# Kernel optimization log

Measured on AMD Instinct MI355X. Metric: run time of the kernel, lower is better.

The kernel has to match this reference:

```python
import jax, jax.numpy as jnp
import numpy as np

HEADS = 8
DIM_HEAD = 64


def setup_inputs() -> dict:
    key = jax.random.key(0)
    ks = jax.random.split(key, 5)
    B, N, C, coor = 2, 2048, 256, 3
    dim_inner = HEADS * DIM_HEAD  # 512
    # weight scale 1/16 ~ 1/sqrt(256) keeps softmax logits in a sane range
    w_scale = 1.0 / 16.0
    return {
        "x": jax.random.normal(ks[0], (B, N, C, coor), dtype=jnp.float32),
        "Wq": jax.random.normal(ks[1], (dim_inner, C), dtype=jnp.float32) * w_scale,
        "Wk": jax.random.normal(ks[2], (dim_inner, C), dtype=jnp.float32) * w_scale,
        "Wv": jax.random.normal(ks[3], (dim_inner, C), dtype=jnp.float32) * w_scale,
        "Wo": jax.random.normal(ks[4], (C, dim_inner), dtype=jnp.float32) * w_scale,
    }


def _split_heads(t, B, N, coor):
    # b n (h d) c -> b h n (d c)
    t = t.reshape(B, N, HEADS, DIM_HEAD, coor)
    t = t.transpose(0, 2, 1, 3, 4)
    return t.reshape(B, HEADS, N, DIM_HEAD * coor)


def reference(x, Wq, Wk, Wv, Wo):
    B, N, C, coor = x.shape
    # VNLinear: einsum('... i c, o i -> ... o c')
    q = jnp.einsum('bnic,oi->bnoc', x, Wq)
    k = jnp.einsum('bnic,oi->bnoc', x, Wk)
    v = jnp.einsum('bnic,oi->bnoc', x, Wv)
    q = _split_heads(q, B, N, coor)  # (B, H, N, d*c)
    k = _split_heads(k, B, N, coor)
    v = _split_heads(v, B, N, coor)
    scale = (DIM_HEAD * coor) ** -0.5
    sim = jnp.einsum('bhie,bhje->bhij', q, k) * scale  # (B, H, N, N)
    attn = jax.nn.softmax(sim, axis=-1)
    out = jnp.einsum('bhij,bhje->bhie', attn, v)  # (B, H, N, d*c)
    # b h n (d c) -> b n (h d) c
    out = out.reshape(B, HEADS, N, DIM_HEAD, coor).transpose(0, 2, 1, 3, 4)
    out = out.reshape(B, N, HEADS * DIM_HEAD, coor)
    # to_out VNLinear
    return jnp.einsum('bnic,oi->bnoc', out, Wo)  # (B, N, C, 3)
```

## Files before the change

### kernel.cpp

```cpp
#include <hip/hip_runtime.h>

#define HEADS 8
#define DH 64
#define CO 3
#define E 192
#define NSEQ 2048
#define BATCH 2
#define CIN 256
#define DINNER 512
#define NTOK 4096
#define BHTOT 16

typedef __attribute__((ext_vector_type(8))) short bf16x8;
typedef __attribute__((ext_vector_type(4))) short bf16x4;
typedef __attribute__((ext_vector_type(4))) float f32x4;
typedef __attribute__((ext_vector_type(4))) float float4v;

static __device__ inline short f2bf(float f) {
  union { float f; unsigned u; } v; v.f = f;
  unsigned r = (v.u + 0x7FFFu + ((v.u >> 16) & 1u)) >> 16;
  return (short)r;
}

static __device__ inline float bf2f(short s) {
  union { unsigned u; float f; } a;
  a.u = ((unsigned)(unsigned short)s) << 16;
  return a.f;
}

static __device__ inline void load_lds16(const short* g, short* l) {
  __builtin_amdgcn_global_load_lds(
      (const __attribute__((address_space(1))) void*)g,
      (__attribute__((address_space(3))) void*)l, 16, 0, 0);
}


__global__ __launch_bounds__(256) void prep(const float* __restrict__ x,
                                            const float* __restrict__ Wq,
                                            const float* __restrict__ Wk,
                                            const float* __restrict__ Wv,
                                            const float* __restrict__ Wo,
                                            short* __restrict__ xcp,
                                            short* __restrict__ wqkvp,
                                            short* __restrict__ wop) {
  int tid = threadIdx.x;
  if (blockIdx.x < 256) {
    __shared__ short st[12288];
    int mt = blockIdx.x;
    const float* xb = x + (size_t)mt * 12288;
#pragma unroll
    for (int r = 0; r < 12; r++) {
      int idx4 = r * 256 + tid;
      float4v v = *(const float4v*)(xb + idx4 * 4);
#pragma unroll
      for (int e = 0; e < 4; e++) {
        int fp = idx4 * 4 + e;
        int ti = fp / 3, c = fp - ti * 3;
        int tl = ti >> 8, i = ti & 255;
        int ks = i >> 5, qd = (i >> 3) & 3, j = i & 7;
        st[c * 4096 + ks * 512 + (qd * 16 + tl) * 8 + j] = f2bf(v[e]);
      }
    }
    __syncthreads();
    short* dst = xcp;
#pragma unroll
    for (int rep = 0; rep < 6; rep++) {
      int g = rep * 256 + tid;
      int c = g >> 9, rem = g & 511;
      *(bf16x8*)(dst + ((size_t)(c * 256 + mt) * 8) * 512 + rem * 8) =
          *(const bf16x8*)&st[c * 4096 + rem * 8];
    }
    return;
  }
  int idx = (blockIdx.x - 256) * 256 + tid;
  const float qscale = 0.07216878364870323f * 1.4426950408889634f;
  if (idx < 1536 * 256) {
    int o = idx >> 8, i = idx & 255;
    float v;
    if (o < 512) v = Wq[idx] * qscale;
    else if (o < 1024) v = Wk[idx - 512 * 256];
    else v = Wv[idx - 1024 * 256];
    int nt = o >> 4, ln = o & 15, ks = i >> 5, qd = (i >> 3) & 3, j = i & 7;
    wqkvp[((size_t)(nt * 8 + ks)) * 512 + (qd * 16 + ln) * 8 + j] = f2bf(v);
  } else {
    int j0 = idx - 1536 * 256;
    if (j0 < 256 * 512) {
      int o2 = j0 >> 9, i = j0 & 511;
      int nt = o2 >> 4, ln = o2 & 15, ks = i >> 5, qd = (i >> 3) & 3, j = i & 7;
      wop[((size_t)(nt * 16 + ks)) * 512 + (qd * 16 + ln) * 8 + j] = f2bf(Wo[j0]);
    }
  }
}

__global__ __launch_bounds__(256, 4) void qkv_gemm(const short* __restrict__ xcp,
                                                   const short* __restrict__ wqkvp,
                                                   short* __restrict__ qp,
                                                   short* __restrict__ kp,
                                                   short* __restrict__ vp) {
  __shared__ __align__(16) short pool[17408];
  int c = blockIdx.z, ntb = blockIdx.x, mtb = blockIdx.y;
  int tid = threadIdx.x, wave = tid >> 6, lane = tid & 63;
  int ln = lane & 15, quad = lane >> 4;
  int wm = wave >> 1, wn = wave & 1;

  const short* gA = xcp + ((size_t)(c * 256 + mtb * 8) * 8) * 512;
  const short* gB = wqkvp + ((size_t)(ntb * 8) * 8) * 512;

  f32x4 acc[4][4] = {};
#pragma unroll
  for (int i = 0; i < 2; i++) {
    int q = tid + 256 * i, mf = q >> 6, l = q & 63;
    load_lds16(gA + (size_t)(mf * 8) * 512 + l * 8, pool + q * 8);
  }
  for (int ks = 0; ks < 8; ks++) {
    int b = ks & 1;
    __syncthreads();
    if (ks < 7) {
#pragma unroll
      for (int i = 0; i < 2; i++) {
        int q = tid + 256 * i, mf = q >> 6, l = q & 63;
        load_lds16(gA + (size_t)(mf * 8 + ks + 1) * 512 + l * 8,
                   pool + (b ^ 1) * 4096 + q * 8);
      }
    }
    const short* As = pool + b * 4096;
    bf16x8 af[4], bfr[4];
#pragma unroll
    for (int j = 0; j < 4; j++)
      bfr[j] = *(const bf16x8*)(gB + (size_t)((wn * 4 + j) * 8 + ks) * 512 + lane * 8);
#pragma unroll
    for (int i = 0; i < 4; i++) af[i] = *(const bf16x8*)&As[(wm * 4 + i) * 512 + lane * 8];
#pragma unroll
    for (int i = 0; i < 4; i++)
#pragma unroll
      for (int j = 0; j < 4; j++)
        acc[i][j] = __builtin_amdgcn_mfma_f32_16x16x32_bf16(af[i], bfr[j], acc[i][j], 0, 0, 0);
  }

  int mat = ntb >> 2;
  int b0 = mtb >> 4;
  if (mat < 2) {
    __syncthreads();
    short* tp = pool;
#pragma unroll
    for (int i = 0; i < 4; i++)
#pragma unroll
      for (int j = 0; j < 4; j++)
#pragma unroll
        for (int jj = 0; jj < 4; jj++)
          tp[(wm * 64 + i * 16 + quad * 4 + jj) * 136 + wn * 64 + j * 16 + ln] =
              f2bf(acc[i][j][jj]);
    __syncthreads();
    short* dst = (mat == 0) ? qp : kp;
    int h0 = (ntb & 3) * 2;
#pragma unroll
    for (int rep = 0; rep < 8; rep++) {
      int gi = rep * 256 + tid;
      int l2 = gi & 15, qd = (gi >> 4) & 3, nf2 = (gi >> 6) & 3,
          esp = (gi >> 8) & 1, hh = (gi >> 9) & 1, kt2 = gi >> 10;
      int tl = kt2 * 64 + nf2 * 16 + l2;
      bf16x8 val = *(const bf16x8*)&tp[tl * 136 + hh * 64 + (esp * 4 + qd) * 8];
      int bhx = b0 * 8 + h0 + hh;
      int kt = (mtb * 2 + kt2) & 31;
      int es = c * 2 + esp;
      size_t off = (((size_t)((bhx * 32 + kt) * 24) + es * 4 + nf2) * 64 +
                    (size_t)(qd * 16 + l2)) * 8;
      *(bf16x8*)(dst + off) = val;
    }
  } else {
#pragma unroll
    for (int i = 0; i < 4; i++) {
      int kt = (mtb * 2 + wm) & 31;
      int ks2 = (i >> 1) & 1;
      int qd2 = (i * 2 + (quad >> 1)) & 3;
#pragma unroll
      for (int j = 0; j < 4; j++) {
        int o = ntb * 128 + wn * 64 + j * 16 + ln;
        int oo = o & 511, h = oo >> 6, d = oo & 63;
        int ef = c * 4 + (d >> 4), l2v = d & 15;
        int bhx = b0 * 8 + h;
        size_t off = ((size_t)((bhx * 32 + kt) * 24 + ks2 * 12 + ef)) * 512 +
                     (qd2 * 16 + l2v) * 8 + (quad & 1) * 4;
        bf16x4 val = { f2bf(acc[i][j][0]), f2bf(acc[i][j][1]),
                       f2bf(acc[i][j][2]), f2bf(acc[i][j][3]) };
        *(bf16x4*)(vp + off) = val;
      }
    }
  }
}

__global__ __launch_bounds__(256, 2) void attn(const short* __restrict__ qp,
                                               const short* __restrict__ kp,
                                               const short* __restrict__ vp,
                                               short* __restrict__ opart,
                                               float* __restrict__ lpart) {
  __shared__ __align__(16) short pool[33792];
  int pair = blockIdx.x, qt = blockIdx.y;
  int bh = pair & 15, kh = pair >> 4;
  int tid = threadIdx.x, wave = tid >> 6, lane = tid & 63;
  int ln = lane & 15, quad = lane >> 4;
  short* Kl = pool;
  short* Vl = pool + 12288;
  short* Pl = pool + 24576;

  bf16x8 qf[2][6];
#pragma unroll
  for (int rg = 0; rg < 2; rg++) {
    int fi = wave * 2 + rg;
    const short* qb = qp +
        ((size_t)(bh * 32 + qt * 2 + (fi >> 2)) * 24 + (fi & 3)) * 512 + lane * 8;
#pragma unroll
    for (int es = 0; es < 6; es++) qf[rg][es] = *(const bf16x8*)(qb + es * 2048);
  }

  float l_r[2][4] = {};
  f32x4 acc[2][12] = {};
  const short* gKb = kp + (size_t)(bh * 32 + kh * 16) * 12288;
  const short* gVb = vp + (size_t)(bh * 32 + kh * 16) * 12288;

  for (int kt = 0; kt < 16; kt++) {
    const short* gK = gKb + (size_t)kt * 12288;
    const short* gV = gVb + (size_t)kt * 12288;
#pragma unroll
    for (int i = 0; i < 6; i++) {
      load_lds16(gK + (i * 256 + tid) * 8, Kl + (i * 256 + tid) * 8);
      load_lds16(gV + (i * 256 + tid) * 8, Vl + (i * 256 + tid) * 8);
    }
    __syncthreads();

    f32x4 s[2][4];
#pragma unroll
    for (int nf = 0; nf < 4; nf++) {
      f32x4 a0 = {}, a1 = {};
#pragma unroll
      for (int es = 0; es < 6; es++) {
        bf16x8 kf = *(const bf16x8*)&Kl[(es * 4 + nf) * 512 + lane * 8];
        a0 = __builtin_amdgcn_mfma_f32_16x16x32_bf16(qf[0][es], kf, a0, 0, 0, 0);
        a1 = __builtin_amdgcn_mfma_f32_16x16x32_bf16(qf[1][es], kf, a1, 0, 0, 0);
      }
      s[0][nf] = a0; s[1][nf] = a1;
    }

#pragma unroll
    for (int rg = 0; rg < 2; rg++)
#pragma unroll
      for (int jj = 0; jj < 4; jj++)
#pragma unroll
        for (int nf = 0; nf < 4; nf++) {
          float p = __builtin_amdgcn_exp2f(s[rg][nf][jj]);
          union { float f; unsigned u; } v; v.f = p;
          Pl[((wave * 2 + rg) * 16 + quad * 4 + jj) * 72 + nf * 16 + ln] =
              (short)((v.u + 0x8000u) >> 16);
          l_r[rg][jj] += p;
        }

    bf16x8 pa[2][2];
#pragma unroll
    for (int rg = 0; rg < 2; rg++) {
      const short* pb = &Pl[((wave * 2 + rg) * 16 + ln) * 72 + quad * 8];
      pa[rg][0] = *(const bf16x8*)pb;
      pa[rg][1] = *(const bf16x8*)(pb + 32);
    }
#pragma unroll
    for (int ef = 0; ef < 12; ef++) {
      bf16x8 v0 = *(const bf16x8*)&Vl[ef * 512 + lane * 8];
      bf16x8 v1 = *(const bf16x8*)&Vl[(12 + ef) * 512 + lane * 8];
#pragma unroll
      for (int rg = 0; rg < 2; rg++) {
        acc[rg][ef] = __builtin_amdgcn_mfma_f32_16x16x32_bf16(pa[rg][0], v0, acc[rg][ef], 0, 0, 0);
        acc[rg][ef] = __builtin_amdgcn_mfma_f32_16x16x32_bf16(pa[rg][1], v1, acc[rg][ef], 0, 0, 0);
      }
    }
    __syncthreads();
  }

#pragma unroll
  for (int rg = 0; rg < 2; rg++)
#pragma unroll
    for (int jj = 0; jj < 4; jj++)
#pragma unroll
      for (int off = 1; off < 16; off <<= 1)
        l_r[rg][jj] += __shfl_xor(l_r[rg][jj], off, 64);

  short* tp = pool;
#pragma unroll
  for (int rg = 0; rg < 2; rg++)
#pragma unroll
    for (int jj = 0; jj < 4; jj++) {
      int row = (wave * 2 + rg) * 16 + quad * 4 + jj;
#pragma unroll
      for (int ef = 0; ef < 12; ef++)
        tp[row * 200 + ef * 16 + ln] = f2bf(acc[rg][ef][jj]);
    }
  __syncthreads();
  const size_t obase = ((size_t)(kh * 16 + bh) * 2048 + qt * 128) * 192;
#pragma unroll
  for (int rep = 0; rep < 12; rep++) {
    int gi = rep * 256 + tid;
    int row = gi / 24, c8 = gi - row * 24;
    *(bf16x8*)(opart + obase + (size_t)row * 192 + c8 * 8) =
        *(const bf16x8*)&tp[row * 200 + c8 * 8];
  }
  int lb = (kh * 16 + bh) * 2048 + qt * 128;
  if (ln == 0) {
#pragma unroll
    for (int rg = 0; rg < 2; rg++)
#pragma unroll
      for (int jj = 0; jj < 4; jj++)
        lpart[lb + (wave * 2 + rg) * 16 + quad * 4 + jj] = l_r[rg][jj];
  }
}

__global__ __launch_bounds__(256, 4) void out_gemm(const short* __restrict__ opart,
                                                   const float* __restrict__ lpart,
                                                   const short* __restrict__ wop,
                                                   float* __restrict__ out) {
  __shared__ __align__(16) short Al[8192];
  int mtb = blockIdx.x, c = blockIdx.y;
  int tid = threadIdx.x, wave = tid >> 6, lane = tid & 63;
  int ln = lane & 15, quad = lane >> 4;
  const size_t HSTR = (size_t)16 * 2048 * 192;

#pragma unroll
  for (int rep = 0; rep < 4; rep++) {
    int g = rep * 256 + tid;
    int d8 = g & 7, h = (g >> 3) & 7, row16 = g >> 6;
    int t = mtb * 16 + row16, b = t >> 11, n = t & 2047;
    int bh = b * 8 + h;
    size_t src = ((size_t)bh * 2048 + n) * 192 + c * 64 + d8 * 8;
    bf16x8 o1 = *(const bf16x8*)(opart + src);
    bf16x8 o2 = *(const bf16x8*)(opart + HSTR + src);
    float l = lpart[bh * 2048 + n] + lpart[32768 + bh * 2048 + n];
    float inv = 1.f / l;
    bf16x8 r;
#pragma unroll
    for (int j = 0; j < 8; j++) r[j] = f2bf((bf2f(o1[j]) + bf2f(o2[j])) * inv);
    int i0 = h * 64 + d8 * 8;
    int ks = i0 >> 5, qd = d8 & 3;
    *(bf16x8*)&Al[ks * 512 + (qd * 16 + row16) * 8] = r;
  }
  __syncthreads();

  f32x4 acc[4] = {};
  for (int ks = 0; ks < 16; ks++) {
    bf16x8 af = *(const bf16x8*)&Al[ks * 512 + lane * 8];
#pragma unroll
    for (int jf = 0; jf < 4; jf++) {
      int nt = wave * 4 + jf;
      bf16x8 bfr = *(const bf16x8*)(wop + (size_t)(nt * 16 + ks) * 512 + lane * 8);
      acc[jf] = __builtin_amdgcn_mfma_f32_16x16x32_bf16(af, bfr, acc[jf], 0, 0, 0);
    }
  }
#pragma unroll
  for (int jf = 0; jf < 4; jf++) {
    int o2 = (wave * 4 + jf) * 16 + ln;
#pragma unroll
    for (int jj = 0; jj < 4; jj++) {
      int t = mtb * 16 + quad * 4 + jj;
      out[((size_t)t * 256 + o2) * 3 + c] = acc[jf][jj];
    }
  }
}

extern "C" void kernel_launch(void* const* d_in, const int* in_sizes, int n_in,
                              void* d_out, int out_size, void* d_ws, size_t ws_size,
                              hipStream_t stream) {
  const float* x  = (const float*)d_in[0];
  const float* Wq = (const float*)d_in[1];
  const float* Wk = (const float*)d_in[2];
  const float* Wv = (const float*)d_in[3];
  const float* Wo = (const float*)d_in[4];
  float* out = (float*)d_out;

  short* ws    = (short*)d_ws;
  short* xcp   = ws;
  short* wqkvp = xcp + 3 * NTOK * CIN;
  short* wop   = wqkvp + 1536 * 256;
  short* qp    = wop + 256 * 512;
  short* kp    = qp + (size_t)BHTOT * NSEQ * E;
  short* vp    = kp + (size_t)BHTOT * NSEQ * E;
  short* opart = vp + (size_t)BHTOT * NSEQ * E;
  float* lpart = (float*)xcp;

  prep<<<2304, 256, 0, stream>>>(x, Wq, Wk, Wv, Wo, xcp, wqkvp, wop);
  qkv_gemm<<<dim3(12, 32, 3), 256, 0, stream>>>(xcp, wqkvp, qp, kp, vp);
  attn<<<dim3(32, 16), 256, 0, stream>>>(qp, kp, vp, opart, lpart);
  out_gemm<<<dim3(256, 3), 256, 0, stream>>>(opart, lpart, wop, out);
}
```

Baseline: 162.7 us.

## Double-buffer K/V tiles in LDS with half-size 32-key steps

The attention kernel splits each 64-key K/V tile into two 32-key halves and double-buffers them in LDS. The next half is prefetched while the current one is computed, replacing the load-sync-compute-sync pattern with one barrier per step. This aims to hide global-to-LDS load latency, at the cost of twice as many loop iterations and barriers and smaller MFMA batches per step. The P staging buffer shrinks, so total LDS drops slightly.

New measurement: 164.4 us. About the same (+1.0%).

```diff
diff --git a/kernel.cpp b/kernel.cpp
--- a/kernel.cpp
+++ b/kernel.cpp
@@ -194,13 +194,11 @@
                                                const short* __restrict__ vp,
                                                short* __restrict__ opart,
                                                float* __restrict__ lpart) {
-  __shared__ __align__(16) short pool[33792];
+  __shared__ __align__(16) short pool[29696];
   int pair = blockIdx.x, qt = blockIdx.y;
   int bh = pair & 15, kh = pair >> 4;
   int tid = threadIdx.x, wave = tid >> 6, lane = tid & 63;
   int ln = lane & 15, quad = lane >> 4;
-  short* Kl = pool;
-  short* Vl = pool + 12288;
   short* Pl = pool + 24576;
 
   bf16x8 qf[2][6];
@@ -218,27 +216,39 @@
   const short* gKb = kp + (size_t)(bh * 32 + kh * 16) * 12288;
   const short* gVb = vp + (size_t)(bh * 32 + kh * 16) * 12288;
 
-  for (int kt = 0; kt < 16; kt++) {
-    const short* gK = gKb + (size_t)kt * 12288;
-    const short* gV = gVb + (size_t)kt * 12288;
-#pragma unroll
-    for (int i = 0; i < 6; i++) {
-      load_lds16(gK + (i * 256 + tid) * 8, Kl + (i * 256 + tid) * 8);
-      load_lds16(gV + (i * 256 + tid) * 8, Vl + (i * 256 + tid) * 8);
-    }
-    __syncthreads();
-
-    f32x4 s[2][4];
-#pragma unroll
-    for (int nf = 0; nf < 4; nf++) {
-      f32x4 a0 = {}, a1 = {};
-#pragma unroll
-      for (int es = 0; es < 6; es++) {
-        bf16x8 kf = *(const bf16x8*)&Kl[(es * 4 + nf) * 512 + lane * 8];
-        a0 = __builtin_amdgcn_mfma_f32_16x16x32_bf16(qf[0][es], kf, a0, 0, 0, 0);
-        a1 = __builtin_amdgcn_mfma_f32_16x16x32_bf16(qf[1][es], kf, a1, 0, 0, 0);
+  auto stage = [&](int k32, int buf) {
+    const short* g64K = gKb + (size_t)(k32 >> 1) * 12288;
+    const short* g64V = gVb + (size_t)(k32 >> 1) * 12288;
+    int half = k32 & 1;
+    short* Kd = pool + buf * 6144;
+    short* Vd = pool + 12288 + buf * 6144;
+#pragma unroll
+    for (int i = 0; i < 3; i++) {
+      int q = i * 256 + tid;
+      int f = q >> 6, l = q & 63;
+      int es = f >> 1, nfl = f & 1;
+      load_lds16(g64K + (size_t)(es * 4 + half * 2 + nfl) * 512 + l * 8, Kd + q * 8);
+      load_lds16(g64V + (size_t)(half * 12 + f) * 512 + l * 8, Vd + q * 8);
+    }
+  };
+
+  stage(0, 0);
+  for (int kt = 0; kt < 32; kt++) {
+    int b = kt & 1;
+    __syncthreads();
+    if (kt < 31) stage(kt + 1, b ^ 1);
+    const short* Kl = pool + b * 6144;
+    const short* Vl = pool + 12288 + b * 6144;
+
+    f32x4 s[2][2] = {};
+#pragma unroll
+    for (int es = 0; es < 6; es++) {
+#pragma unroll
+      for (int nfl = 0; nfl < 2; nfl++) {
+        bf16x8 kf = *(const bf16x8*)&Kl[(es * 2 + nfl) * 512 + lane * 8];
+        s[0][nfl] = __builtin_amdgcn_mfma_f32_16x16x32_bf16(qf[0][es], kf, s[0][nfl], 0, 0, 0);
+        s[1][nfl] = __builtin_amdgcn_mfma_f32_16x16x32_bf16(qf[1][es], kf, s[1][nfl], 0, 0, 0);
       }
-      s[0][nf] = a0; s[1][nf] = a1;
     }
 
 #pragma unroll
@@ -246,32 +256,25 @@
 #pragma unroll
       for (int jj = 0; jj < 4; jj++)
 #pragma unroll
-        for (int nf = 0; nf < 4; nf++) {
-          float p = __builtin_amdgcn_exp2f(s[rg][nf][jj]);
+        for (int nfl = 0; nfl < 2; nfl++) {
+          float p = __builtin_amdgcn_exp2f(s[rg][nfl][jj]);
           union { float f; unsigned u; } v; v.f = p;
-          Pl[((wave * 2 + rg) * 16 + quad * 4 + jj) * 72 + nf * 16 + ln] =
+          Pl[((wave * 2 + rg) * 16 + quad * 4 + jj) * 40 + nfl * 16 + ln] =
               (short)((v.u + 0x8000u) >> 16);
           l_r[rg][jj] += p;
         }
 
-    bf16x8 pa[2][2];
-#pragma unroll
-    for (int rg = 0; rg < 2; rg++) {
-      const short* pb = &Pl[((wave * 2 + rg) * 16 + ln) * 72 + quad * 8];
-      pa[rg][0] = *(const bf16x8*)pb;
-      pa[rg][1] = *(const bf16x8*)(pb + 32);
-    }
+    bf16x8 pa[2];
+#pragma unroll
+    for (int rg = 0; rg < 2; rg++)
+      pa[rg] = *(const bf16x8*)&Pl[((wave * 2 + rg) * 16 + ln) * 40 + quad * 8];
+
 #pragma unroll
     for (int ef = 0; ef < 12; ef++) {
       bf16x8 v0 = *(const bf16x8*)&Vl[ef * 512 + lane * 8];
-      bf16x8 v1 = *(const bf16x8*)&Vl[(12 + ef) * 512 + lane * 8];
-#pragma unroll
-      for (int rg = 0; rg < 2; rg++) {
-        acc[rg][ef] = __builtin_amdgcn_mfma_f32_16x16x32_bf16(pa[rg][0], v0, acc[rg][ef], 0, 0, 0);
-        acc[rg][ef] = __builtin_amdgcn_mfma_f32_16x16x32_bf16(pa[rg][1], v1, acc[rg][ef], 0, 0, 0);
-      }
-    }
-    __syncthreads();
+      acc[0][ef] = __builtin_amdgcn_mfma_f32_16x16x32_bf16(pa[0], v0, acc[0][ef], 0, 0, 0);
+      acc[1][ef] = __builtin_amdgcn_mfma_f32_16x16x32_bf16(pa[1], v0, acc[1][ef], 0, 0, 0);
+    }
   }
 
 #pragma unroll
@@ -282,6 +285,7 @@
       for (int off = 1; off < 16; off <<= 1)
         l_r[rg][jj] += __shfl_xor(l_r[rg][jj], off, 64);
 
+  __syncthreads();
   short* tp = pool;
 #pragma unroll
   for (int rg = 0; rg < 2; rg++)
```
